# Optimization experiments

Hardware: AMD Instinct MI355X
Metric: run time of the kernel (lower is better)

Reference implementation:

```python
import jax, jax.numpy as jnp
import numpy as np

N_NODES = 100000
N_EDGES = 1600000
D = 128  # 2 * config.out_channels with config.out_channels = 64


def setup_inputs() -> dict:
    key = jax.random.key(0)
    k1, k2, k3, k4 = jax.random.split(key, 4)
    x_in = jax.random.normal(k1, (N_NODES, D), dtype=jnp.float32)
    x_out = jax.random.normal(k2, (N_NODES, D), dtype=jnp.float32)
    edge_index = jax.random.randint(k3, (2, N_EDGES), 0, N_NODES, dtype=jnp.int64)
    # nn.Bilinear(D, D, 1, bias=False) weight: [out_features=1, D, D]
    W = jax.random.normal(k4, (1, D, D), dtype=jnp.float32) * (1.0 / np.sqrt(D))
    return {"x_in": x_in, "x_out": x_out, "edge_index": edge_index, "W": W}


def reference(x_in, x_out, edge_index, W):
    # Gather edge endpoint features (irregular access)
    a = x_out[edge_index[0]]          # [E, D]
    b = x_in[edge_index[1]]           # [E, D]
    # Bilinear form with single output: value_e = a_e^T W0 b_e
    W0 = W[0]                         # [D, D]
    aW = a @ W0                       # [E, D]
    value = jnp.sum(aW * b, axis=-1)  # [E]
    return jax.nn.sigmoid(value)
```

## Files before the change

kernel.cpp:

```cpp
#include <hip/hip_runtime.h>
#include <hip/hip_fp16.h>
#include <math.h>

#define D 128
#define CONV_BLOCKS 1024

typedef _Float16 f16x8 __attribute__((ext_vector_type(8)));
typedef float    f32x4 __attribute__((ext_vector_type(4)));
typedef _Float16 h2_t  __attribute__((ext_vector_type(2)));

__device__ __forceinline__ float dot2acc(unsigned ua, unsigned ub, float c) {
#if __has_builtin(__builtin_amdgcn_fdot2)
  return __builtin_amdgcn_fdot2(__builtin_bit_cast(h2_t, ua),
                                __builtin_bit_cast(h2_t, ub), c, false);
#else
  __half2 a = __builtin_bit_cast(__half2, ua);
  __half2 b = __builtin_bit_cast(__half2, ub);
  float2 fa = __half22float2(a), fb = __half22float2(b);
  return fmaf(fa.x, fb.x, fmaf(fa.y, fb.y, c));
#endif
}

__device__ __forceinline__ unsigned pack2(float x, float y) {
  __half2 h;
  h.x = __float2half_rn(x);
  h.y = __float2half_rn(y);
  return __builtin_bit_cast(unsigned, h);
}

__global__ __launch_bounds__(256) void prep_kernel(
    const float* __restrict__ Xout, const float* __restrict__ Xin,
    const float* __restrict__ W, __half* __restrict__ Yh,
    __half* __restrict__ Xh, int N, int gemm_blocks)
{
  __shared__ __align__(16) __half sA[128 * 128];
  __shared__ __align__(16) __half sB[128 * 128];

  const int tid = threadIdx.x;

  if ((int)blockIdx.x >= gemm_blocks) {
    const int cb = blockIdx.x - gemm_blocks;
    const int n4 = N * (D / 4);
    const int stride = CONV_BLOCKS * 256 * 4;
    for (int base = (cb * 256 + tid) * 4; base < n4; base += stride) {
      float4 v[4];
      #pragma unroll
      for (int j = 0; j < 4; j++)
        if (base + j < n4) v[j] = ((const float4*)Xin)[base + j];
      #pragma unroll
      for (int j = 0; j < 4; j++)
        if (base + j < n4) {
          uint2 u;
          u.x = pack2(v[j].x, v[j].y);
          u.y = pack2(v[j].z, v[j].w);
          ((uint2*)Xh)[base + j] = u;
        }
    }
    return;
  }

  const int row0 = blockIdx.x * 128;

  #pragma unroll
  for (int i = 0; i < 16; i++) {
    int idx = tid + i * 256;
    int q   = idx & 31;
    int r   = idx >> 5;
    int gr  = row0 + r;
    float4 v = make_float4(0.f, 0.f, 0.f, 0.f);
    if (gr < N) v = *(const float4*)(Xout + (size_t)gr * D + q * 4);
    uint2 u;
    u.x = pack2(v.x, v.y);
    u.y = pack2(v.z, v.w);
    int g   = q >> 1;
    int sub = q & 1;
    int off = r * 128 + (((g + r) & 15) << 3) + (sub << 2);
    *(uint2*)(sA + off) = u;
  }
  #pragma unroll
  for (int i = 0; i < 64; i++) {
    int o = tid + i * 256;
    int k = o >> 7;
    int n = o & 127;
    __half h = __float2half_rn(W[o]);
    int gk = k >> 3;
    sB[n * 128 + (((gk + n) & 15) << 3) + (k & 7)] = h;
  }
  __syncthreads();

  const int wave = tid >> 6;
  const int lane = tid & 63;
  const int m    = lane & 15;
  const int quad = lane >> 4;

  f32x4 acc[2][8];
  #pragma unroll
  for (int rt = 0; rt < 2; rt++)
    #pragma unroll
    for (int ct = 0; ct < 8; ct++)
      acc[rt][ct] = (f32x4){0.f, 0.f, 0.f, 0.f};

  #pragma unroll
  for (int ks = 0; ks < 4; ks++) {
    const int g = ks * 4 + quad;
    f16x8 bfrag[8];
    #pragma unroll
    for (int ct = 0; ct < 8; ct++) {
      int n = ct * 16 + m;
      bfrag[ct] = *(const f16x8*)(sB + n * 128 + (((g + n) & 15) << 3));
    }
    #pragma unroll
    for (int rt = 0; rt < 2; rt++) {
      int r = wave * 32 + rt * 16 + m;
      f16x8 afrag = *(const f16x8*)(sA + r * 128 + (((g + r) & 15) << 3));
      #pragma unroll
      for (int ct = 0; ct < 8; ct++)
        acc[rt][ct] = __builtin_amdgcn_mfma_f32_16x16x32_f16(
            afrag, bfrag[ct], acc[rt][ct], 0, 0, 0);
    }
  }

  __syncthreads();
  __half* sC = sA;
  #pragma unroll
  for (int rt = 0; rt < 2; rt++)
    #pragma unroll
    for (int reg = 0; reg < 4; reg++) {
      int r = wave * 32 + rt * 16 + quad * 4 + reg;
      #pragma unroll
      for (int ct = 0; ct < 8; ct++)
        sC[r * 128 + ct * 16 + m] = __float2half_rn(acc[rt][ct][reg]);
    }
  __syncthreads();
  #pragma unroll
  for (int i = 0; i < 8; i++) {
    int idx = tid + i * 256;
    int r   = idx >> 4;
    int gq  = idx & 15;
    int gr  = row0 + r;
    if (gr < N)
      *(uint4*)(Yh + (size_t)gr * D + gq * 8) = *(const uint4*)(sC + r * 128 + gq * 8);
  }
}

__global__ __launch_bounds__(256) void edge_dot2_kernel(
    const __half* __restrict__ Yh, const __half* __restrict__ Xh,
    const int* __restrict__ idx, float* __restrict__ out, int E)
{
  long long gid = (long long)blockIdx.x * 256 + threadIdx.x;
  int slot = (int)(gid >> 4);
  int l    = (int)(gid & 15);
  int e0 = slot * 2;
  if (e0 >= E) return;
  int e1 = e0 + 1;
  bool has1 = (e1 < E);

  int s0 = idx[e0];
  int d0 = idx[E + e0];
  int s1 = has1 ? idx[e1] : s0;
  int d1 = has1 ? idx[E + e1] : d0;

  uint4 a0 = ((const uint4*)(Yh + (size_t)s0 * D))[l];
  uint4 b0 = ((const uint4*)(Xh + (size_t)d0 * D))[l];
  uint4 a1 = ((const uint4*)(Yh + (size_t)s1 * D))[l];
  uint4 b1 = ((const uint4*)(Xh + (size_t)d1 * D))[l];

  float p = 0.f, q = 0.f;
  p = dot2acc(a0.x, b0.x, p);  q = dot2acc(a1.x, b1.x, q);
  p = dot2acc(a0.y, b0.y, p);  q = dot2acc(a1.y, b1.y, q);
  p = dot2acc(a0.z, b0.z, p);  q = dot2acc(a1.z, b1.z, q);
  p = dot2acc(a0.w, b0.w, p);  q = dot2acc(a1.w, b1.w, q);

  p += __shfl_xor(p, 8);  q += __shfl_xor(q, 8);
  p += __shfl_xor(p, 4);  q += __shfl_xor(q, 4);
  p += __shfl_xor(p, 2);  q += __shfl_xor(q, 2);
  p += __shfl_xor(p, 1);  q += __shfl_xor(q, 1);

  if (l == 0) {
    float2 o;
    o.x = 1.0f / (1.0f + __expf(-p));
    o.y = 1.0f / (1.0f + __expf(-q));
    if (has1) *(float2*)(out + e0) = o;
    else      out[e0] = o.x;
  }
}

__global__ __launch_bounds__(256) void edge_bilinear_direct_kernel(
    const float* __restrict__ Xout, const float* __restrict__ Xin,
    const float* __restrict__ W, const int* __restrict__ idx,
    float* __restrict__ out, int E)
{
  long long gid = (long long)blockIdx.x * 256 + threadIdx.x;
  int e = (int)(gid >> 6);
  if (e >= E) return;
  int l = (int)(gid & 63);

  int src = idx[e];
  int dst = idx[E + e];
  const float* a = Xout + (size_t)src * D;
  const float* b = Xin  + (size_t)dst * D;

  float s = 0.f;
  #pragma unroll
  for (int kk = 0; kk < 2; kk++) {
    int k = l + kk * 64;
    float ak = a[k];
    float t = 0.f;
    #pragma unroll 8
    for (int j = 0; j < D; j++) t = fmaf(W[(size_t)k * D + j], b[j], t);
    s = fmaf(ak, t, s);
  }
  #pragma unroll
  for (int off = 32; off >= 1; off >>= 1) s += __shfl_xor(s, off);
  if (l == 0) out[e] = 1.0f / (1.0f + __expf(-s));
}

extern "C" void kernel_launch(void* const* d_in, const int* in_sizes, int n_in,
                              void* d_out, int out_size, void* d_ws, size_t ws_size,
                              hipStream_t stream) {
  const float* x_in  = (const float*)d_in[0];
  const float* x_out = (const float*)d_in[1];
  const int*   eidx  = (const int*)d_in[2];
  const float* W     = (const float*)d_in[3];
  float* out = (float*)d_out;

  const int N = in_sizes[0] / D;
  const int E = in_sizes[2] / 2;

  const size_t half_rows = (size_t)N * D * sizeof(__half);

  if (ws_size >= 2 * half_rows) {
    __half* Yh = (__half*)d_ws;
    __half* Xh = (__half*)((char*)d_ws + half_rows);

    int gemm_blocks = (N + 127) / 128;
    dim3 g1(gemm_blocks + CONV_BLOCKS);
    prep_kernel<<<g1, 256, 0, stream>>>(x_out, x_in, W, Yh, Xh, N, gemm_blocks);

    long long slots = (E + 1) / 2;
    long long total = slots * 16;
    dim3 g2((unsigned)((total + 255) / 256));
    edge_dot2_kernel<<<g2, 256, 0, stream>>>(Yh, Xh, eidx, out, E);
  } else {
    long long total = (long long)E * 64;
    dim3 g((unsigned)((total + 255) / 256));
    edge_bilinear_direct_kernel<<<g, 256, 0, stream>>>(x_out, x_in, W, eidx, out, E);
  }
}
```

Baseline: 254.3 us.

## Pre-transpose W to fp16 once, shrink GEMM tiles, process four edges per slot

A small kernel now converts and transposes W to fp16 once, so the GEMM blocks read B fragments straight from global/L2 instead of each block converting all of W into shared memory. The GEMM tile drops to 64 rows with less shared memory, giving more blocks and higher occupancy, and the number of conversion blocks doubles. The edge kernel handles four edges per 16-lane group, raising memory-level parallelism for the gathers and writing float4 outputs. The cost is an extra launch and repeated global reads of W fragments in every block.

```diff
diff --git a/kernel.cpp b/kernel.cpp
--- a/kernel.cpp
+++ b/kernel.cpp
@@ -3,7 +3,9 @@
 #include <math.h>
 
 #define D 128
-#define CONV_BLOCKS 1024
+#define GM 64
+#define CONV_BLOCKS 2048
+#define CONV_BLOCKS_OLD 1024
 
 typedef _Float16 f16x8 __attribute__((ext_vector_type(8)));
 typedef float    f32x4 __attribute__((ext_vector_type(4)));
@@ -28,6 +30,121 @@
   return __builtin_bit_cast(unsigned, h);
 }
 
+__global__ __launch_bounds__(256) void wt_kernel(const float* __restrict__ W,
+                                                 __half* __restrict__ WhT) {
+  const int n  = blockIdx.x * 16 + (threadIdx.x >> 4);
+  const int k0 = (threadIdx.x & 15) * 8;
+  float w[8];
+  #pragma unroll
+  for (int kk = 0; kk < 8; kk++) w[kk] = W[(k0 + kk) * D + n];
+  uint4 u;
+  u.x = pack2(w[0], w[1]); u.y = pack2(w[2], w[3]);
+  u.z = pack2(w[4], w[5]); u.w = pack2(w[6], w[7]);
+  *(uint4*)(WhT + n * D + k0) = u;
+}
+
+__global__ __launch_bounds__(256) void prep2_kernel(
+    const float* __restrict__ Xout, const float* __restrict__ Xin,
+    const __half* __restrict__ WhT, __half* __restrict__ Yh,
+    __half* __restrict__ Xh, int N, int gemm_blocks)
+{
+  __shared__ __align__(16) __half sA[GM * D];
+
+  const int tid = threadIdx.x;
+
+  if ((int)blockIdx.x >= gemm_blocks) {
+    const int cb = blockIdx.x - gemm_blocks;
+    const int n4 = N * (D / 4);
+    const int stride = CONV_BLOCKS * 256 * 4;
+    for (int base = (cb * 256 + tid) * 4; base < n4; base += stride) {
+      float4 v[4];
+      #pragma unroll
+      for (int j = 0; j < 4; j++)
+        if (base + j < n4) v[j] = ((const float4*)Xin)[base + j];
+      #pragma unroll
+      for (int j = 0; j < 4; j++)
+        if (base + j < n4) {
+          uint2 u;
+          u.x = pack2(v[j].x, v[j].y);
+          u.y = pack2(v[j].z, v[j].w);
+          ((uint2*)Xh)[base + j] = u;
+        }
+    }
+    return;
+  }
+
+  const int row0 = blockIdx.x * GM;
+
+  float4 v[8];
+  #pragma unroll
+  for (int i = 0; i < 4; i++) {
+    int gi = tid + i * 256;
+    int r = gi >> 4, q = gi & 15;
+    int gr = row0 + r;
+    if (gr < N) {
+      const float4* s = (const float4*)(Xout + (size_t)gr * D + q * 8);
+      v[2*i]   = s[0];
+      v[2*i+1] = s[1];
+    } else {
+      v[2*i]   = make_float4(0.f, 0.f, 0.f, 0.f);
+      v[2*i+1] = make_float4(0.f, 0.f, 0.f, 0.f);
+    }
+  }
+  #pragma unroll
+  for (int i = 0; i < 4; i++) {
+    int gi = tid + i * 256;
+    int r = gi >> 4, q = gi & 15;
+    uint4 u;
+    u.x = pack2(v[2*i].x,   v[2*i].y);
+    u.y = pack2(v[2*i].z,   v[2*i].w);
+    u.z = pack2(v[2*i+1].x, v[2*i+1].y);
+    u.w = pack2(v[2*i+1].z, v[2*i+1].w);
+    *(uint4*)(sA + r * D + ((q ^ (r & 7)) << 3)) = u;
+  }
+  __syncthreads();
+
+  const int lane = tid & 63, wave = tid >> 6;
+  const int m = lane & 15, quad = lane >> 4;
+  const int rloc = wave * 16 + m;
+
+  f32x4 acc[8];
+  #pragma unroll
+  for (int ct = 0; ct < 8; ct++) acc[ct] = (f32x4){0.f, 0.f, 0.f, 0.f};
+
+  #pragma unroll
+  for (int ks = 0; ks < 4; ks++) {
+    const int g = ks * 4 + quad;
+    f16x8 bfrag[8];
+    #pragma unroll
+    for (int ct = 0; ct < 8; ct++)
+      bfrag[ct] = *(const f16x8*)(WhT + (size_t)(ct * 16 + m) * D + g * 8);
+    f16x8 afrag = *(const f16x8*)(sA + rloc * D + ((g ^ (rloc & 7)) << 3));
+    #pragma unroll
+    for (int ct = 0; ct < 8; ct++)
+      acc[ct] = __builtin_amdgcn_mfma_f32_16x16x32_f16(
+          afrag, bfrag[ct], acc[ct], 0, 0, 0);
+  }
+
+  __syncthreads();
+  __half* sC = sA;
+  #pragma unroll
+  for (int ct = 0; ct < 8; ct++)
+    #pragma unroll
+    for (int reg = 0; reg < 4; reg++) {
+      int r = wave * 16 + quad * 4 + reg;
+      sC[r * D + ct * 16 + m] = __float2half_rn(acc[ct][reg]);
+    }
+  __syncthreads();
+  #pragma unroll
+  for (int i = 0; i < 4; i++) {
+    int gi = tid + i * 256;
+    int r = gi >> 4, q = gi & 15;
+    int gr = row0 + r;
+    if (gr < N)
+      *(uint4*)(Yh + (size_t)gr * D + q * 8) = *(const uint4*)(sC + r * D + q * 8);
+  }
+}
+
 __global__ __launch_bounds__(256) void prep_kernel(
     const float* __restrict__ Xout, const float* __restrict__ Xin,
     const float* __restrict__ W, __half* __restrict__ Yh,
@@ -41,7 +158,7 @@
   if ((int)blockIdx.x >= gemm_blocks) {
     const int cb = blockIdx.x - gemm_blocks;
     const int n4 = N * (D / 4);
-    const int stride = CONV_BLOCKS * 256 * 4;
+    const int stride = CONV_BLOCKS_OLD * 256 * 4;
     for (int base = (cb * 256 + tid) * 4; base < n4; base += stride) {
       float4 v[4];
       #pragma unroll
@@ -143,45 +260,60 @@
   }
 }
 
-__global__ __launch_bounds__(256) void edge_dot2_kernel(
+__global__ __launch_bounds__(256) void edge_dot4_kernel(
     const __half* __restrict__ Yh, const __half* __restrict__ Xh,
     const int* __restrict__ idx, float* __restrict__ out, int E)
 {
   long long gid = (long long)blockIdx.x * 256 + threadIdx.x;
   int slot = (int)(gid >> 4);
   int l    = (int)(gid & 15);
-  int e0 = slot * 2;
+  int e0 = slot * 4;
   if (e0 >= E) return;
-  int e1 = e0 + 1;
-  bool has1 = (e1 < E);
-
-  int s0 = idx[e0];
-  int d0 = idx[E + e0];
-  int s1 = has1 ? idx[e1] : s0;
-  int d1 = has1 ? idx[E + e1] : d0;
-
-  uint4 a0 = ((const uint4*)(Yh + (size_t)s0 * D))[l];
-  uint4 b0 = ((const uint4*)(Xh + (size_t)d0 * D))[l];
-  uint4 a1 = ((const uint4*)(Yh + (size_t)s1 * D))[l];
-  uint4 b1 = ((const uint4*)(Xh + (size_t)d1 * D))[l];
-
-  float p = 0.f, q = 0.f;
-  p = dot2acc(a0.x, b0.x, p);  q = dot2acc(a1.x, b1.x, q);
-  p = dot2acc(a0.y, b0.y, p);  q = dot2acc(a1.y, b1.y, q);
-  p = dot2acc(a0.z, b0.z, p);  q = dot2acc(a1.z, b1.z, q);
-  p = dot2acc(a0.w, b0.w, p);  q = dot2acc(a1.w, b1.w, q);
-
-  p += __shfl_xor(p, 8);  q += __shfl_xor(q, 8);
-  p += __shfl_xor(p, 4);  q += __shfl_xor(q, 4);
-  p += __shfl_xor(p, 2);  q += __shfl_xor(q, 2);
-  p += __shfl_xor(p, 1);  q += __shfl_xor(q, 1);
+
+  int s[4], d[4];
+  #pragma unroll
+  for (int i = 0; i < 4; i++) {
+    int e = e0 + i; if (e > E - 1) e = E - 1;
+    s[i] = idx[e];
+    d[i] = idx[E + e];
+  }
+  uint4 a[4], b[4];
+  #pragma unroll
+  for (int i = 0; i < 4; i++) a[i] = ((const uint4*)(Yh + (size_t)s[i] * D))[l];
+  #pragma unroll
+  for (int i = 0; i < 4; i++) b[i] = ((const uint4*)(Xh + (size_t)d[i] * D))[l];
+
+  float p[4];
+  #pragma unroll
+  for (int i = 0; i < 4; i++) {
+    float t = 0.f;
+    t = dot2acc(a[i].x, b[i].x, t);
+    t = dot2acc(a[i].y, b[i].y, t);
+    t = dot2acc(a[i].z, b[i].z, t);
+    t = dot2acc(a[i].w, b[i].w, t);
+    p[i] = t;
+  }
+  #pragma unroll
+  for (int i = 0; i < 4; i++) {
+    p[i] += __shfl_xor(p[i], 8);
+    p[i] += __shfl_xor(p[i], 4);
+    p[i] += __shfl_xor(p[i], 2);
+    p[i] += __shfl_xor(p[i], 1);
+  }
 
   if (l == 0) {
-    float2 o;
-    o.x = 1.0f / (1.0f + __expf(-p));
-    o.y = 1.0f / (1.0f + __expf(-q));
-    if (has1) *(float2*)(out + e0) = o;
-    else      out[e0] = o.x;
+    float4 o;
+    o.x = 1.0f / (1.0f + __expf(-p[0]));
+    o.y = 1.0f / (1.0f + __expf(-p[1]));
+    o.z = 1.0f / (1.0f + __expf(-p[2]));
+    o.w = 1.0f / (1.0f + __expf(-p[3]));
+    if (e0 + 3 < E) {
+      *(float4*)(out + e0) = o;
+    } else {
+      out[e0] = o.x;
+      if (e0 + 1 < E) out[e0 + 1] = o.y;
+      if (e0 + 2 < E) out[e0 + 2] = o.z;
+    }
   }
 }
 
@@ -228,19 +360,35 @@
   const int E = in_sizes[2] / 2;
 
   const size_t half_rows = (size_t)N * D * sizeof(__half);
-
-  if (ws_size >= 2 * half_rows) {
+  const size_t wht_bytes = (size_t)D * D * sizeof(__half);
+
+  if (ws_size >= 2 * half_rows + wht_bytes) {
+    __half* Yh  = (__half*)d_ws;
+    __half* Xh  = (__half*)((char*)d_ws + half_rows);
+    __half* WhT = (__half*)((char*)d_ws + 2 * half_rows);
+
+    wt_kernel<<<dim3(8), 256, 0, stream>>>(W, WhT);
+
+    int gemm_blocks = (N + GM - 1) / GM;
+    dim3 g1(gemm_blocks + CONV_BLOCKS);
+    prep2_kernel<<<g1, 256, 0, stream>>>(x_out, x_in, WhT, Yh, Xh, N, gemm_blocks);
+
+    long long slots = ((long long)E + 3) / 4;
+    long long total = slots * 16;
+    dim3 g2((unsigned)((total + 255) / 256));
+    edge_dot4_kernel<<<g2, 256, 0, stream>>>(Yh, Xh, eidx, out, E);
+  } else if (ws_size >= 2 * half_rows) {
     __half* Yh = (__half*)d_ws;
     __half* Xh = (__half*)((char*)d_ws + half_rows);
 
     int gemm_blocks = (N + 127) / 128;
-    dim3 g1(gemm_blocks + CONV_BLOCKS);
+    dim3 g1(gemm_blocks + CONV_BLOCKS_OLD);
     prep_kernel<<<g1, 256, 0, stream>>>(x_out, x_in, W, Yh, Xh, N, gemm_blocks);
 
-    long long slots = (E + 1) / 2;
+    long long slots = ((long long)E + 3) / 4;
     long long total = slots * 16;
     dim3 g2((unsigned)((total + 255) / 256));
-    edge_dot2_kernel<<<g2, 256, 0, stream>>>(Yh, Xh, eidx, out, E);
+    edge_dot4_kernel<<<g2, 256, 0, stream>>>(Yh, Xh, eidx, out, E);
   } else {
     long long total = (long long)E * 64;
     dim3 g((unsigned)((total + 255) / 256));
```

After: 261.9 us. 3.0% more time.

## Halve GEMM row tile to 64, switch sA to XOR swizzle, double conversion blocks

Applied to the files above, without the earlier changes.

The prep kernel's GEMM tile shrinks from 128 to 64 rows per block, so each wave computes one 16-row tile instead of two. This uses less shared memory and fewer accumulator registers, and doubles the number of GEMM blocks for better occupancy and load balance. Xout is loaded as two float4 per thread and stored as uint4 into an XOR-swizzled layout, and the fp16 conversion blocks for Xin double to 2048. The cost is that every block still converts the full 128x128 W to fp16 in shared memory, so that per-block overhead now repeats across twice as many GEMM blocks.

```diff
diff --git a/kernel.cpp b/kernel.cpp
--- a/kernel.cpp
+++ b/kernel.cpp
@@ -3,7 +3,8 @@
 #include <math.h>
 
 #define D 128
-#define CONV_BLOCKS 1024
+#define GM 64
+#define CONV_BLOCKS 2048
 
 typedef _Float16 f16x8 __attribute__((ext_vector_type(8)));
 typedef float    f32x4 __attribute__((ext_vector_type(4)));
@@ -28,18 +29,19 @@
   return __builtin_bit_cast(unsigned, h);
 }
 
-__global__ __launch_bounds__(256) void prep_kernel(
+__global__ __launch_bounds__(256) void prep3_kernel(
     const float* __restrict__ Xout, const float* __restrict__ Xin,
     const float* __restrict__ W, __half* __restrict__ Yh,
     __half* __restrict__ Xh, int N, int gemm_blocks)
 {
-  __shared__ __align__(16) __half sA[128 * 128];
-  __shared__ __align__(16) __half sB[128 * 128];
+  __shared__ __align__(16) __half sA[GM * D];
+  __shared__ __align__(16) __half sB[D * D];
 
   const int tid = threadIdx.x;
-
-  if ((int)blockIdx.x >= gemm_blocks) {
-    const int cb = blockIdx.x - gemm_blocks;
+  const int bid = blockIdx.x;
+
+  if (bid >= gemm_blocks) {
+    const int cb = bid - gemm_blocks;
     const int n4 = N * (D / 4);
     const int stride = CONV_BLOCKS * 256 * 4;
     for (int base = (cb * 256 + tid) * 4; base < n4; base += stride) {
@@ -59,24 +61,35 @@
     return;
   }
 
-  const int row0 = blockIdx.x * 128;
-
-  #pragma unroll
-  for (int i = 0; i < 16; i++) {
-    int idx = tid + i * 256;
-    int q   = idx & 31;
-    int r   = idx >> 5;
-    int gr  = row0 + r;
-    float4 v = make_float4(0.f, 0.f, 0.f, 0.f);
-    if (gr < N) v = *(const float4*)(Xout + (size_t)gr * D + q * 4);
-    uint2 u;
-    u.x = pack2(v.x, v.y);
-    u.y = pack2(v.z, v.w);
-    int g   = q >> 1;
-    int sub = q & 1;
-    int off = r * 128 + (((g + r) & 15) << 3) + (sub << 2);
-    *(uint2*)(sA + off) = u;
-  }
+  const int row0 = bid * GM;
+
+  float4 v[8];
+  #pragma unroll
+  for (int i = 0; i < 4; i++) {
+    int gi = tid + i * 256;
+    int r = gi >> 4, q = gi & 15;
+    int gr = row0 + r;
+    if (gr < N) {
+      const float4* s = (const float4*)(Xout + (size_t)gr * D + q * 8);
+      v[2*i]   = s[0];
+      v[2*i+1] = s[1];
+    } else {
+      v[2*i]   = make_float4(0.f, 0.f, 0.f, 0.f);
+      v[2*i+1] = make_float4(0.f, 0.f, 0.f, 0.f);
+    }
+  }
+  #pragma unroll
+  for (int i = 0; i < 4; i++) {
+    int gi = tid + i * 256;
+    int r = gi >> 4, q = gi & 15;
+    uint4 u;
+    u.x = pack2(v[2*i].x,   v[2*i].y);
+    u.y = pack2(v[2*i].z,   v[2*i].w);
+    u.z = pack2(v[2*i+1].x, v[2*i+1].y);
+    u.w = pack2(v[2*i+1].z, v[2*i+1].w);
+    *(uint4*)(sA + r * D + ((q ^ (r & 7)) << 3)) = u;
+  }
+
   #pragma unroll
   for (int i = 0; i < 64; i++) {
     int o = tid + i * 256;
@@ -88,17 +101,13 @@
   }
   __syncthreads();
 
-  const int wave = tid >> 6;
-  const int lane = tid & 63;
-  const int m    = lane & 15;
-  const int quad = lane >> 4;
-
-  f32x4 acc[2][8];
-  #pragma unroll
-  for (int rt = 0; rt < 2; rt++)
-    #pragma unroll
-    for (int ct = 0; ct < 8; ct++)
-      acc[rt][ct] = (f32x4){0.f, 0.f, 0.f, 0.f};
+  const int lane = tid & 63, wave = tid >> 6;
+  const int m = lane & 15, quad = lane >> 4;
+  const int rloc = wave * 16 + m;
+
+  f32x4 acc[8];
+  #pragma unroll
+  for (int ct = 0; ct < 8; ct++) acc[ct] = (f32x4){0.f, 0.f, 0.f, 0.f};
 
   #pragma unroll
   for (int ks = 0; ks < 4; ks++) {
@@ -109,37 +118,30 @@
       int n = ct * 16 + m;
       bfrag[ct] = *(const f16x8*)(sB + n * 128 + (((g + n) & 15) << 3));
     }
+    f16x8 afrag = *(const f16x8*)(sA + rloc * D + ((g ^ (rloc & 7)) << 3));
     #pragma unroll
-    for (int rt = 0; rt < 2; rt++) {
-      int r = wave * 32 + rt * 16 + m;
-      f16x8 afrag = *(const f16x8*)(sA + r * 128 + (((g + r) & 15) << 3));
-      #pragma unroll
-      for (int ct = 0; ct < 8; ct++)
-        acc[rt][ct] = __builtin_amdgcn_mfma_f32_16x16x32_f16(
-            afrag, bfrag[ct], acc[rt][ct], 0, 0, 0);
-    }
+    for (int ct = 0; ct < 8; ct++)
+      acc[ct] = __builtin_amdgcn_mfma_f32_16x16x32_f16(
+          afrag, bfrag[ct], acc[ct], 0, 0, 0);
   }
 
   __syncthreads();
   __half* sC = sA;
   #pragma unroll
-  for (int rt = 0; rt < 2; rt++)
+  for (int ct = 0; ct < 8; ct++)
     #pragma unroll
     for (int reg = 0; reg < 4; reg++) {
-      int r = wave * 32 + rt * 16 + quad * 4 + reg;
-      #pragma unroll
-      for (int ct = 0; ct < 8; ct++)
-        sC[r * 128 + ct * 16 + m] = __float2half_rn(acc[rt][ct][reg]);
+      int r = wave * 16 + quad * 4 + reg;
+      sC[r * D + ct * 16 + m] = __float2half_rn(acc[ct][reg]);
     }
   __syncthreads();
   #pragma unroll
-  for (int i = 0; i < 8; i++) {
-    int idx = tid + i * 256;
-    int r   = idx >> 4;
-    int gq  = idx & 15;
-    int gr  = row0 + r;
+  for (int i = 0; i < 4; i++) {
+    int gi = tid + i * 256;
+    int r = gi >> 4, q = gi & 15;
+    int gr = row0 + r;
     if (gr < N)
-      *(uint4*)(Yh + (size_t)gr * D + gq * 8) = *(const uint4*)(sC + r * 128 + gq * 8);
+      *(uint4*)(Yh + (size_t)gr * D + q * 8) = *(const uint4*)(sC + r * D + q * 8);
   }
 }
 
@@ -233,11 +235,11 @@
     __half* Yh = (__half*)d_ws;
     __half* Xh = (__half*)((char*)d_ws + half_rows);
 
-    int gemm_blocks = (N + 127) / 128;
+    int gemm_blocks = (N + GM - 1) / GM;
     dim3 g1(gemm_blocks + CONV_BLOCKS);
-    prep_kernel<<<g1, 256, 0, stream>>>(x_out, x_in, W, Yh, Xh, N, gemm_blocks);
-
-    long long slots = (E + 1) / 2;
+    prep3_kernel<<<g1, 256, 0, stream>>>(x_out, x_in, W, Yh, Xh, N, gemm_blocks);
+
+    long long slots = ((long long)E + 1) / 2;
     long long total = slots * 16;
     dim3 g2((unsigned)((total + 255) / 256));
     edge_dot2_kernel<<<g2, 256, 0, stream>>>(Yh, Xh, eidx, out, E);
```

New measurement: 247.2 us. 1.03x faster.
